# Kernel tuning notes

Measured on AMD Instinct MI355X. Metric: run time of the kernel, lower is better.

The kernel has to match this reference:

```python
import jax, jax.numpy as jnp
import numpy as np

B, S, LC, DIM, H, FFN = 1, 3600, 512, 1536, 12, 8960
HD = DIM // H          # 128
GRID = (4, 30, 30)     # f*h*w == S
K_LEN = 9900           # hardcoded k_lens in SelfAttention.forward
EPS = 1e-6

def _rope_axis_angles(n_pos, dim):
    inv = 1.0 / np.power(10000.0, np.arange(0, dim, 2, dtype=np.float64) / dim)
    return np.outer(np.arange(n_pos), inv)

def _build_rope(grid, head_dim):
    c = head_dim // 2                      # 64
    c1, c2 = c - 2 * (c // 3), c // 3      # 22, 21 (Wan 3D rope split)
    f, h, w = grid
    af = _rope_axis_angles(f, 2 * c1)
    ah = _rope_axis_angles(h, 2 * c2)
    aw = _rope_axis_angles(w, 2 * c2)
    ang = np.concatenate([
        np.broadcast_to(af[:, None, None, :], (f, h, w, c1)),
        np.broadcast_to(ah[None, :, None, :], (f, h, w, c2)),
        np.broadcast_to(aw[None, None, :, :], (f, h, w, c2)),
    ], axis=-1).reshape(f * h * w, c)
    return np.cos(ang).astype(np.float32), np.sin(ang).astype(np.float32)

def setup_inputs():
    key = jax.random.key(0)
    ks = iter(jax.random.split(key, 40))
    cos, sin = _build_rope(GRID, HD)
    inp = {
        'x': jax.random.normal(next(ks), (B, S, DIM), dtype=jnp.float32),
        'context': jax.random.normal(next(ks), (B, LC, DIM), dtype=jnp.float32),
        't_mod': 0.1 * jax.random.normal(next(ks), (B, 6, DIM), dtype=jnp.float32),
        'rope_cos': jnp.asarray(cos), 'rope_sin': jnp.asarray(sin),
        'modulation': jax.random.normal(next(ks), (1, 6, DIM), dtype=jnp.float32) / DIM ** 0.5,
    }
    for p in ('sa', 'ca'):
        for w in ('q', 'k', 'v', 'o'):
            inp[p + '_' + w + 'w'] = 0.02 * jax.random.normal(next(ks), (DIM, DIM), dtype=jnp.float32)
            inp[p + '_' + w + 'b'] = jnp.zeros((DIM,), jnp.float32)
        inp[p + '_nq'] = jnp.ones((DIM,), jnp.float32)
        inp[p + '_nk'] = jnp.ones((DIM,), jnp.float32)
    inp['n3_w'] = jnp.ones((DIM,), jnp.float32)
    inp['n3_b'] = jnp.zeros((DIM,), jnp.float32)
    inp['ffn_w1'] = 0.02 * jax.random.normal(next(ks), (DIM, FFN), dtype=jnp.float32)
    inp['ffn_b1'] = jnp.zeros((FFN,), jnp.float32)
    inp['ffn_w2'] = 0.02 * jax.random.normal(next(ks), (FFN, DIM), dtype=jnp.float32)
    inp['ffn_b2'] = jnp.zeros((DIM,), jnp.float32)
    return inp

def _rms(x, w):
    x32 = x.astype(jnp.float32)
    n = x32 * jax.lax.rsqrt(jnp.mean(x32 * x32, axis=-1, keepdims=True) + EPS)
    return n.astype(x.dtype) * w

def _ln(x, w=None, b=None):
    mu = jnp.mean(x, axis=-1, keepdims=True)
    var = jnp.mean(jnp.square(x - mu), axis=-1, keepdims=True)
    y = (x - mu) * jax.lax.rsqrt(var + EPS)
    return y if w is None else y * w + b

def _rope(x, cos, sin):
    b, s, h, d = x.shape
    x2 = x.reshape(b, s, h, d // 2, 2)
    xe, xo = x2[..., 0], x2[..., 1]
    c, sn = cos[None, :, None, :], sin[None, :, None, :]
    return jnp.stack([xe * c - xo * sn, xe * sn + xo * c], axis=-1).reshape(b, s, h, d)

def _attn(q, k, v, k_len=None):
    # q,k,v: [B,S,H,D]
    scores = jnp.einsum('bqhd,bkhd->bhqk', q, k) * (q.shape[-1] ** -0.5)
    if k_len is not None:
        mask = jnp.arange(k.shape[1]) < k_len
        scores = jnp.where(mask[None, None, None, :], scores, jnp.finfo(scores.dtype).min)
    return jnp.einsum('bhqk,bkhd->bqhd', jax.nn.softmax(scores, axis=-1), v)

def reference(x, context, t_mod, rope_cos, rope_sin, modulation,
              sa_qw, sa_qb, sa_kw, sa_kb, sa_vw, sa_vb, sa_ow, sa_ob, sa_nq, sa_nk,
              ca_qw, ca_qb, ca_kw, ca_kb, ca_vw, ca_vb, ca_ow, ca_ob, ca_nq, ca_nk,
              n3_w, n3_b, ffn_w1, ffn_b1, ffn_w2, ffn_b2):
    mod = modulation + t_mod                      # [B,6,DIM]
    sh_msa, sc_msa, g_msa, sh_mlp, sc_mlp, g_mlp = [mod[:, i:i + 1] for i in range(6)]
    b = x.shape[0]
    # --- self-attention with AdaLN modulate + 3D RoPE + k_lens mask ---
    h = _ln(x) * (1 + sc_msa) + sh_msa
    q = _rms(h @ sa_qw + sa_qb, sa_nq).reshape(b, -1, H, HD)
    k = _rms(h @ sa_kw + sa_kb, sa_nk).reshape(b, -1, H, HD)
    v = (h @ sa_vw + sa_vb).reshape(b, -1, H, HD)
    a = _attn(_rope(q, rope_cos, rope_sin), _rope(k, rope_cos, rope_sin), v, k_len=K_LEN)
    x = x + g_msa * (a.reshape(b, -1, DIM) @ sa_ow + sa_ob)
    # --- cross-attention ---
    hc = _ln(x, n3_w, n3_b)
    q = _rms(hc @ ca_qw + ca_qb, ca_nq).reshape(b, -1, H, HD)
    k = _rms(context @ ca_kw + ca_kb, ca_nk).reshape(b, -1, H, HD)
    v = (context @ ca_vw + ca_vb).reshape(b, -1, H, HD)
    x = x + (_attn(q, k, v).reshape(b, -1, DIM) @ ca_ow + ca_ob)
    # --- gated FFN with AdaLN modulate ---
    h = _ln(x) * (1 + sc_mlp) + sh_mlp
    h = jax.nn.gelu(h @ ffn_w1 + ffn_b1, approximate=True) @ ffn_w2 + ffn_b2
    return x + g_mlp * h
```

## Files before the change

kernel.cpp:

```cpp
#include <hip/hip_runtime.h>
#include <cstdint>

#define S_LEN 3600
#define DMODEL 1536
#define LCTX 512
#define NH 12
#define HDIM 128
#define FFND 8960
#define SPAD_SELF 3616

typedef short v8s __attribute__((ext_vector_type(8)));
typedef float v4f __attribute__((ext_vector_type(4)));
typedef unsigned short u16b;
typedef unsigned int u32b;

__device__ __forceinline__ u16b f2b(float f){
  union { float f; u32b i; } x; x.f = f;
  u32b r = x.i + 0x7fffu + ((x.i >> 16) & 1u);
  return (u16b)(r >> 16);
}

__device__ __forceinline__ int swz4(int row){ return (row ^ (row >> 2)) & 3; }

__global__ void add_vec(const float* __restrict__ a, const float* __restrict__ b,
                        float* __restrict__ o, int n){
  int i = blockIdx.x * 256 + threadIdx.x;
  if (i < n) o[i] = a[i] + b[i];
}

__global__ void f2b_kernel(const float* __restrict__ in, u16b* __restrict__ out, int n){
  int i = blockIdx.x * 256 + threadIdx.x;
  if (i < n) out[i] = f2b(in[i]);
}

struct WJob { const float* W; u16b* WT; int K; int N; int t0; };
struct WJobs { WJob j[10]; };

__global__ __launch_bounds__(256) void wconv(WJobs jobs){
  __shared__ float tile[32][33];
  int b = blockIdx.x;
  int ji = 0;
  #pragma unroll
  for (int i = 0; i < 10; ++i) if (b >= jobs.j[i].t0) ji = i;
  WJob jb = jobs.j[ji];
  int rel = b - jb.t0;
  int ntn = jb.N / 32;
  int k0 = (rel / ntn) * 32, n0 = (rel % ntn) * 32;
  int tx = threadIdx.x & 31, ty = threadIdx.x >> 5;
  #pragma unroll
  for (int r = ty; r < 32; r += 8) tile[r][tx] = jb.W[(size_t)(k0 + r) * jb.N + n0 + tx];
  __syncthreads();
  #pragma unroll
  for (int r = ty; r < 32; r += 8) jb.WT[(size_t)(n0 + r) * jb.K + k0 + tx] = f2b(tile[tx][r]);
}

__global__ __launch_bounds__(256) void vtrans(const u16b* __restrict__ V,
                                              u16b* __restrict__ Vt,
                                              int S, int Spad){
  __shared__ u16b t[32][136];
  int h = blockIdx.y, kb = blockIdx.x * 32, tid = threadIdx.x;
  int row = tid >> 3, ch = tid & 7;
  int key = kb + row;
  if (key < S){
    float4 a = *(const float4*)(V + (size_t)key * DMODEL + h * HDIM + ch * 16);
    float4 b = *(const float4*)(V + (size_t)key * DMODEL + h * HDIM + ch * 16 + 8);
    *(float4*)&t[row][ch * 16] = a;
    *(float4*)&t[row][ch * 16 + 8] = b;
  } else {
    float4 z = {0.f, 0.f, 0.f, 0.f};
    *(float4*)&t[row][ch * 16] = z;
    *(float4*)&t[row][ch * 16 + 8] = z;
  }
  __syncthreads();
  int hd = tid >> 1, kc = (tid & 1) * 16;
  u16b* dst = Vt + ((size_t)h * HDIM + hd) * Spad + kb + kc;
  #pragma unroll
  for (int e = 0; e < 16; e += 2){
    u32b pk = ((u32b)t[kc + e][hd]) | (((u32b)t[kc + e + 1][hd]) << 16);
    *(u32b*)(dst + e) = pk;
  }
}

__global__ __launch_bounds__(256) void ln_mod(const float* __restrict__ X,
                                              const float* __restrict__ gamma,
                                              const float* __restrict__ beta,
                                              float gadd, u16b* __restrict__ out){
  int row = blockIdx.x;
  const float* xr = X + (size_t)row * DMODEL;
  int tid = threadIdx.x;
  float v[6]; float s1 = 0.f, s2 = 0.f;
  #pragma unroll
  for (int j = 0; j < 6; ++j){ v[j] = xr[tid + j * 256]; s1 += v[j]; s2 += v[j] * v[j]; }
  #pragma unroll
  for (int o = 1; o < 64; o <<= 1){ s1 += __shfl_xor(s1, o); s2 += __shfl_xor(s2, o); }
  __shared__ float red[8];
  int wid = tid >> 6, lane = tid & 63;
  if (!lane){ red[wid * 2] = s1; red[wid * 2 + 1] = s2; }
  __syncthreads();
  s1 = red[0] + red[2] + red[4] + red[6];
  s2 = red[1] + red[3] + red[5] + red[7];
  float mu = s1 / DMODEL;
  float var = s2 / DMODEL - mu * mu;
  float rstd = rsqrtf(var + 1e-6f);
  #pragma unroll
  for (int j = 0; j < 6; ++j){
    int c = tid + j * 256;
    float g = gamma[c] + gadd;
    float b = beta[c];
    out[(size_t)row * DMODEL + c] = f2b((v[j] - mu) * rstd * g + b);
  }
}

__global__ __launch_bounds__(256) void rms_rope(const float* __restrict__ X,
                                                const float* __restrict__ w,
                                                const float* __restrict__ cosT,
                                                const float* __restrict__ sinT,
                                                u16b* __restrict__ out){
  int row = blockIdx.x;
  const float* xr = X + (size_t)row * DMODEL;
  int tid = threadIdx.x;
  float2 v[3]; float ss = 0.f;
  #pragma unroll
  for (int j = 0; j < 3; ++j){
    v[j] = *(const float2*)(xr + 2 * (tid + j * 256));
    ss += v[j].x * v[j].x + v[j].y * v[j].y;
  }
  #pragma unroll
  for (int o = 1; o < 64; o <<= 1) ss += __shfl_xor(ss, o);
  __shared__ float red[4];
  int wid = tid >> 6, lane = tid & 63;
  if (!lane) red[wid] = ss;
  __syncthreads();
  ss = red[0] + red[1] + red[2] + red[3];
  float rstd = rsqrtf(ss / DMODEL + 1e-6f);
  #pragma unroll
  for (int j = 0; j < 3; ++j){
    int p = tid + j * 256;
    float xe = v[j].x * rstd * w[2 * p];
    float xo = v[j].y * rstd * w[2 * p + 1];
    float oe, oo;
    if (cosT){
      int d = p & 63;
      float c = cosT[row * 64 + d], sn = sinT[row * 64 + d];
      oe = xe * c - xo * sn; oo = xe * sn + xo * c;
    } else { oe = xe; oo = xo; }
    u32b packed = ((u32b)f2b(oe)) | (((u32b)f2b(oo)) << 16);
    *(u32b*)(out + (size_t)row * DMODEL + 2 * p) = packed;
  }
}

template<int EPI>
__global__ __launch_bounds__(256, 2) void gemm_bt(
    const u16b* __restrict__ A, const u16b* __restrict__ BT,
    const float* __restrict__ bias, const float* __restrict__ res,
    const float* __restrict__ gate, float* __restrict__ outF,
    u16b* __restrict__ outB, int M, int N, int K)
{
  __shared__ u16b Al[128 * 32];
  __shared__ u16b Bl[128 * 32];
  const int tid = threadIdx.x, lane = tid & 63, wid = tid >> 6;
  const int bm = blockIdx.x * 128, bn = blockIdx.y * 128;
  const int wm = (wid >> 1) * 64, wn = (wid & 1) * 64;
  v4f acc[4][4] = {};
  const int g0 = tid, g1 = tid + 256;
  const int r0 = g0 >> 2, c0 = g0 & 3, r1 = g1 >> 2, c1 = g1 & 3;
  const size_t a_off0 = (size_t)min(bm + r0, M - 1) * K + c0 * 8;
  const size_t a_off1 = (size_t)min(bm + r1, M - 1) * K + c1 * 8;
  const size_t b_off0 = (size_t)(bn + r0) * K + c0 * 8;
  const size_t b_off1 = (size_t)(bn + r1) * K + c1 * 8;
  char* Ab = (char*)Al; char* Bb = (char*)Bl;
  const int wA0 = r0 * 64 + ((c0 ^ swz4(r0)) * 16);
  const int wA1 = r1 * 64 + ((c1 ^ swz4(r1)) * 16);
  float4 ra0, ra1, rb0, rb1;
  auto ldg = [&](int k0){
    ra0 = *(const float4*)(A + a_off0 + k0);
    ra1 = *(const float4*)(A + a_off1 + k0);
    rb0 = *(const float4*)(BT + b_off0 + k0);
    rb1 = *(const float4*)(BT + b_off1 + k0);
  };
  auto stw = [&](){
    *(float4*)(Ab + wA0) = ra0; *(float4*)(Ab + wA1) = ra1;
    *(float4*)(Bb + wA0) = rb0; *(float4*)(Bb + wA1) = rb1;
  };
  const int nt = K / 32;
  ldg(0); stw(); __syncthreads();
  const int chk = lane >> 4, qr = lane & 15;
  for (int t = 0; t < nt; ++t){
    if (t + 1 < nt) ldg((t + 1) * 32);
    v8s af[4], bfr[4];
    #pragma unroll
    for (int f = 0; f < 4; ++f){
      int rowa = wm + f * 16 + qr;
      af[f] = *(const v8s*)(Ab + rowa * 64 + ((chk ^ swz4(rowa)) * 16));
      int rowb = wn + f * 16 + qr;
      bfr[f] = *(const v8s*)(Bb + rowb * 64 + ((chk ^ swz4(rowb)) * 16));
    }
    #pragma unroll
    for (int i = 0; i < 4; ++i)
      #pragma unroll
      for (int j = 0; j < 4; ++j)
        acc[i][j] = __builtin_amdgcn_mfma_f32_16x16x32_bf16(af[i], bfr[j], acc[i][j], 0, 0, 0);
    __syncthreads();
    if (t + 1 < nt){ stw(); __syncthreads(); }
  }
  const int rr = lane >> 4;
  #pragma unroll
  for (int i = 0; i < 4; ++i){
    #pragma unroll
    for (int j = 0; j < 4; ++j){
      int n = bn + wn + j * 16 + qr;
      float bv = bias ? bias[n] : 0.f;
      float gv = (EPI == 2 && gate) ? gate[n] : 1.f;
      #pragma unroll
      for (int r = 0; r < 4; ++r){
        int m = bm + wm + i * 16 + rr * 4 + r;
        if (m < M){
          float val = acc[i][j][r] + bv;
          size_t idx = (size_t)m * N + n;
          if (EPI == 0) outB[idx] = f2b(val);
          else if (EPI == 1) outF[idx] = val;
          else if (EPI == 2) outF[idx] = res[idx] + gv * val;
          else {
            float t3 = val * val * val;
            float th = tanhf(0.7978845608028654f * (val + 0.044715f * t3));
            outB[idx] = f2b(0.5f * val * (1.f + th));
          }
        }
      }
    }
  }
}

__global__ __launch_bounds__(256, 2) void flash_attn(
    const u16b* __restrict__ Q, const u16b* __restrict__ Kp,
    const u16b* __restrict__ Vt, u16b* __restrict__ O,
    int Sq, int Sk, int Spad)
{
  __shared__ u16b Klds[32 * 128];
  __shared__ u16b Vlds[128 * 32];
  __shared__ u16b Plds[4 * 16 * 32];
  const int tid = threadIdx.x, lane = tid & 63, wid = tid >> 6;
  const int h = blockIdx.y;
  const int q0 = blockIdx.x * 64 + wid * 16;
  const int qq = lane & 15, cc = lane >> 4;
  char* Kb = (char*)Klds; char* Vb = (char*)Vlds; char* Pb = (char*)Plds;

  v8s qf[4];
  {
    int qrow = min(q0 + qq, Sq - 1);
    const u16b* qp = Q + (size_t)qrow * DMODEL + h * HDIM + cc * 8;
    #pragma unroll
    for (int ks = 0; ks < 4; ++ks) qf[ks] = *(const v8s*)(qp + ks * 32);
  }
  float mrun = -1e30f, lrun = 0.f;
  v4f oacc[8] = {};
  const float scale = 0.08838834764831845f;

  for (int kb0 = 0; kb0 < Sk; kb0 += 32){
    __syncthreads();
    #pragma unroll
    for (int c = 0; c < 2; ++c){
      int g = tid + c * 256;
      int krow = g >> 4, kgc = g & 15;
      int key = min(kb0 + krow, Sk - 1);
      *(float4*)(Kb + krow * 256 + ((kgc ^ (krow & 7)) * 16)) =
          *(const float4*)(Kp + (size_t)key * DMODEL + h * HDIM + kgc * 8);
      int vr = g >> 2, vc = g & 3;
      *(float4*)(Vb + vr * 64 + ((vc ^ swz4(vr)) * 16)) =
          *(const float4*)(Vt + ((size_t)h * HDIM + vr) * Spad + kb0 + vc * 8);
    }
    __syncthreads();

    float s[8];
    #pragma unroll
    for (int sub = 0; sub < 2; ++sub){
      v4f sa = {0.f, 0.f, 0.f, 0.f};
      #pragma unroll
      for (int ks = 0; ks < 4; ++ks){
        int row = sub * 16 + qq;
        v8s kf = *(const v8s*)(Kb + row * 256 + (((ks * 4 + cc) ^ (row & 7)) * 16));
        sa = __builtin_amdgcn_mfma_f32_16x16x32_bf16(kf, qf[ks], sa, 0, 0, 0);
      }
      #pragma unroll
      for (int r = 0; r < 4; ++r) s[sub * 4 + r] = sa[r] * scale;
    }
    if (kb0 + 32 > Sk){
      #pragma unroll
      for (int i = 0; i < 8; ++i){
        int key = kb0 + (i >> 2) * 16 + cc * 4 + (i & 3);
        if (key >= Sk) s[i] = -1e30f;
      }
    }
    float cmax = s[0];
    #pragma unroll
    for (int i = 1; i < 8; ++i) cmax = fmaxf(cmax, s[i]);
    cmax = fmaxf(cmax, __shfl_xor(cmax, 16));
    cmax = fmaxf(cmax, __shfl_xor(cmax, 32));
    float mnew = fmaxf(mrun, cmax);
    float alpha = __expf(mrun - mnew);
    mrun = mnew;
    float p[8]; float csum = 0.f;
    #pragma unroll
    for (int i = 0; i < 8; ++i){ p[i] = __expf(s[i] - mnew); csum += p[i]; }
    csum += __shfl_xor(csum, 16);
    csum += __shfl_xor(csum, 32);
    lrun = lrun * alpha + csum;

    #pragma unroll
    for (int sub = 0; sub < 2; ++sub){
      int key0 = sub * 16 + cc * 4;
      u32b u01 = ((u32b)f2b(p[sub * 4 + 0])) | (((u32b)f2b(p[sub * 4 + 1])) << 16);
      u32b u23 = ((u32b)f2b(p[sub * 4 + 2])) | (((u32b)f2b(p[sub * 4 + 3])) << 16);
      char* base = Pb + wid * 1024 + qq * 64 + (((key0 >> 3) ^ ((qq >> 1) & 3)) * 16) + (key0 & 7) * 2;
      *(u32b*)base = u01;
      *(u32b*)(base + 4) = u23;
    }
    float alr[4];
    #pragma unroll
    for (int r = 0; r < 4; ++r) alr[r] = __shfl(alpha, cc * 4 + r);
    #pragma unroll
    for (int f = 0; f < 8; ++f)
      #pragma unroll
      for (int r = 0; r < 4; ++r) oacc[f][r] *= alr[r];

    v8s pf = *(const v8s*)(Pb + wid * 1024 + qq * 64 + ((cc ^ ((qq >> 1) & 3)) * 16));

    #pragma unroll
    for (int hdb = 0; hdb < 8; ++hdb){
      int row = hdb * 16 + qq;
      v8s vf = *(const v8s*)(Vb + row * 64 + ((cc ^ swz4(row)) * 16));
      oacc[hdb] = __builtin_amdgcn_mfma_f32_16x16x32_bf16(pf, vf, oacc[hdb], 0, 0, 0);
    }
  }

  float linv = 1.f / lrun;
  float lr[4];
  #pragma unroll
  for (int r = 0; r < 4; ++r) lr[r] = __shfl(linv, cc * 4 + r);
  #pragma unroll
  for (int hdb = 0; hdb < 8; ++hdb)
    #pragma unroll
    for (int r = 0; r < 4; ++r){
      int qrow = q0 + cc * 4 + r;
      if (qrow < Sq)
        O[(size_t)qrow * DMODEL + h * HDIM + hdb * 16 + qq] = f2b(oacc[hdb][r] * lr[r]);
    }
}

extern "C" void kernel_launch(void* const* d_in, const int* in_sizes, int n_in,
                              void* d_out, int out_size, void* d_ws, size_t ws_size,
                              hipStream_t stream){
  (void)in_sizes; (void)n_in; (void)out_size; (void)ws_size;
  const float* x     = (const float*)d_in[0];
  const float* ctx   = (const float*)d_in[1];
  const float* t_mod = (const float*)d_in[2];
  const float* ropec = (const float*)d_in[3];
  const float* ropes = (const float*)d_in[4];
  const float* modu  = (const float*)d_in[5];
  const float* sa_qw = (const float*)d_in[6];  const float* sa_qb = (const float*)d_in[7];
  const float* sa_kw = (const float*)d_in[8];  const float* sa_kb = (const float*)d_in[9];
  const float* sa_vw = (const float*)d_in[10]; const float* sa_vb = (const float*)d_in[11];
  const float* sa_ow = (const float*)d_in[12]; const float* sa_ob = (const float*)d_in[13];
  const float* sa_nq = (const float*)d_in[14]; const float* sa_nk = (const float*)d_in[15];
  const float* ca_qw = (const float*)d_in[16]; const float* ca_qb = (const float*)d_in[17];
  const float* ca_kw = (const float*)d_in[18]; const float* ca_kb = (const float*)d_in[19];
  const float* ca_vw = (const float*)d_in[20]; const float* ca_vb = (const float*)d_in[21];
  const float* ca_ow = (const float*)d_in[22]; const float* ca_ob = (const float*)d_in[23];
  const float* ca_nq = (const float*)d_in[24]; const float* ca_nk = (const float*)d_in[25];
  const float* n3w   = (const float*)d_in[26]; const float* n3b   = (const float*)d_in[27];
  const float* fw1   = (const float*)d_in[28]; const float* fb1   = (const float*)d_in[29];
  const float* fw2   = (const float*)d_in[30]; const float* fb2   = (const float*)d_in[31];
  float* out = (float*)d_out;

  char* wsp = (char*)d_ws;
  size_t off = 0;
  auto alloc = [&](size_t b){ void* p = wsp + off; off += (b + 255) & ~(size_t)255; return p; };
  const size_t WW = (size_t)DMODEL * DMODEL * 2;
  float* modc = (float*)alloc(6 * DMODEL * 4);
  u16b* w1T   = (u16b*)alloc((size_t)FFND * DMODEL * 2);
  u16b* w2T   = (u16b*)alloc((size_t)DMODEL * FFND * 2);
  u16b* h_bf  = (u16b*)alloc((size_t)S_LEN * DMODEL * 2);
  float* pre0 = (float*)alloc((size_t)S_LEN * DMODEL * 4);
  size_t region0 = off;
  u16b* sa_qwT = (u16b*)alloc(WW);
  u16b* sa_kwT = (u16b*)alloc(WW);
  u16b* sa_vwT = (u16b*)alloc(WW);
  u16b* sa_owT = (u16b*)alloc(WW);
  u16b* ca_qwT = (u16b*)alloc(WW);
  u16b* ca_kwT = (u16b*)alloc(WW);
  u16b* ca_vwT = (u16b*)alloc(WW);
  u16b* ca_owT = (u16b*)alloc(WW);
  float* x2    = (float*)alloc((size_t)S_LEN * DMODEL * 4);
  float* pre2  = (float*)alloc((size_t)LCTX * DMODEL * 4);
  u16b* qb     = (u16b*)alloc((size_t)S_LEN * DMODEL * 2);
  u16b* kb     = (u16b*)alloc((size_t)S_LEN * DMODEL * 2);
  u16b* vb     = (u16b*)alloc((size_t)S_LEN * DMODEL * 2);
  u16b* ab     = (u16b*)alloc((size_t)S_LEN * DMODEL * 2);
  u16b* ctxb   = (u16b*)alloc((size_t)LCTX * DMODEL * 2);
  u16b* k2b    = (u16b*)alloc((size_t)LCTX * DMODEL * 2);
  u16b* v2b    = (u16b*)alloc((size_t)LCTX * DMODEL * 2);
  u16b* vts    = (u16b*)alloc((size_t)NH * HDIM * SPAD_SELF * 2);
  u16b* vtc    = (u16b*)alloc((size_t)NH * HDIM * LCTX * 2);
  u16b* fmid = (u16b*)(wsp + region0);

  add_vec<<<36, 256, 0, stream>>>(modu, t_mod, modc, 6 * DMODEL);

  WJobs jobs; int t = 0;
  auto addjob = [&](int i, const float* w_, u16b* wt, int K, int N){
    jobs.j[i].W = w_; jobs.j[i].WT = wt; jobs.j[i].K = K; jobs.j[i].N = N; jobs.j[i].t0 = t;
    t += (K / 32) * (N / 32);
  };
  addjob(0, sa_qw, sa_qwT, DMODEL, DMODEL);
  addjob(1, sa_kw, sa_kwT, DMODEL, DMODEL);
  addjob(2, sa_vw, sa_vwT, DMODEL, DMODEL);
  addjob(3, sa_ow, sa_owT, DMODEL, DMODEL);
  addjob(4, ca_qw, ca_qwT, DMODEL, DMODEL);
  addjob(5, ca_kw, ca_kwT, DMODEL, DMODEL);
  addjob(6, ca_vw, ca_vwT, DMODEL, DMODEL);
  addjob(7, ca_ow, ca_owT, DMODEL, DMODEL);
  addjob(8, fw1, w1T, DMODEL, FFND);
  addjob(9, fw2, w2T, FFND, DMODEL);
  wconv<<<t, 256, 0, stream>>>(jobs);

  f2b_kernel<<<(LCTX * DMODEL) / 256, 256, 0, stream>>>(ctx, ctxb, LCTX * DMODEL);

  ln_mod<<<S_LEN, 256, 0, stream>>>(x, modc + DMODEL, modc, 1.f, h_bf);
  dim3 g12(29, 12), g42(4, 12);
  gemm_bt<1><<<g12, 256, 0, stream>>>(h_bf, sa_qwT, sa_qb, nullptr, nullptr, pre0, nullptr, S_LEN, DMODEL, DMODEL);
  gemm_bt<1><<<g12, 256, 0, stream>>>(h_bf, sa_kwT, sa_kb, nullptr, nullptr, x2, nullptr, S_LEN, DMODEL, DMODEL);
  gemm_bt<0><<<g12, 256, 0, stream>>>(h_bf, sa_vwT, sa_vb, nullptr, nullptr, nullptr, vb, S_LEN, DMODEL, DMODEL);
  rms_rope<<<S_LEN, 256, 0, stream>>>(pre0, sa_nq, ropec, ropes, qb);
  rms_rope<<<S_LEN, 256, 0, stream>>>(x2, sa_nk, ropec, ropes, kb);
  vtrans<<<dim3(113, 12), 256, 0, stream>>>(vb, vts, S_LEN, SPAD_SELF);
  flash_attn<<<dim3(57, 12), 256, 0, stream>>>(qb, kb, vts, ab, S_LEN, S_LEN, SPAD_SELF);
  gemm_bt<2><<<g12, 256, 0, stream>>>(ab, sa_owT, sa_ob, x, modc + 2 * DMODEL, x2, nullptr, S_LEN, DMODEL, DMODEL);

  ln_mod<<<S_LEN, 256, 0, stream>>>(x2, n3w, n3b, 0.f, h_bf);
  gemm_bt<1><<<g12, 256, 0, stream>>>(h_bf, ca_qwT, ca_qb, nullptr, nullptr, pre0, nullptr, S_LEN, DMODEL, DMODEL);
  gemm_bt<1><<<g42, 256, 0, stream>>>(ctxb, ca_kwT, ca_kb, nullptr, nullptr, pre2, nullptr, LCTX, DMODEL, DMODEL);
  gemm_bt<0><<<g42, 256, 0, stream>>>(ctxb, ca_vwT, ca_vb, nullptr, nullptr, nullptr, v2b, LCTX, DMODEL, DMODEL);
  rms_rope<<<S_LEN, 256, 0, stream>>>(pre0, ca_nq, nullptr, nullptr, qb);
  rms_rope<<<LCTX, 256, 0, stream>>>(pre2, ca_nk, nullptr, nullptr, k2b);
  vtrans<<<dim3(16, 12), 256, 0, stream>>>(v2b, vtc, LCTX, LCTX);
  flash_attn<<<dim3(57, 12), 256, 0, stream>>>(qb, k2b, vtc, ab, S_LEN, LCTX, LCTX);
  gemm_bt<2><<<g12, 256, 0, stream>>>(ab, ca_owT, ca_ob, x2, nullptr, pre0, nullptr, S_LEN, DMODEL, DMODEL);

  ln_mod<<<S_LEN, 256, 0, stream>>>(pre0, modc + 4 * DMODEL, modc + 3 * DMODEL, 1.f, h_bf);
  gemm_bt<3><<<dim3(29, 70), 256, 0, stream>>>(h_bf, w1T, fb1, nullptr, nullptr, nullptr, fmid, S_LEN, FFND, DMODEL);
  gemm_bt<2><<<g12, 256, 0, stream>>>(fmid, w2T, fb2, pre0, modc + 5 * DMODEL, out, nullptr, S_LEN, DMODEL, FFND);
}
```

Before: 1.104 ms.

## Fuse QKV GEMMs, split-K FFN2, widen flash-attn tiles with prefetch and lazy rescale

The self-attention Q/K/V projections now run as one segmented GEMM over concatenated transposed weights, and the cross-attention K/V projections are merged the same way. The FFN down-projection is split along K into two partial GEMMs followed by a reduce kernel that applies bias, gate and residual, so the narrow N=1536 grid gets more blocks. Flash attention moves to 64-key tiles with register prefetch of the next K/V tile and skips the online-softmax rescale unless the running max grows by more than a threshold. MFMA sections are wrapped in s_setprio, and SPAD is raised to a multiple of 64. These changes add LDS use and a partial-sum buffer, and the lazy rescale trades a little exp headroom for fewer multiplies.

```diff
diff --git a/kernel.cpp b/kernel.cpp
--- a/kernel.cpp
+++ b/kernel.cpp
@@ -7,7 +7,7 @@
 #define NH 12
 #define HDIM 128
 #define FFND 8960
-#define SPAD_SELF 3616
+#define SPAD_SELF 3648
 
 typedef short v8s __attribute__((ext_vector_type(8)));
 typedef float v4f __attribute__((ext_vector_type(4)));
@@ -154,7 +154,93 @@
     const u16b* __restrict__ A, const u16b* __restrict__ BT,
     const float* __restrict__ bias, const float* __restrict__ res,
     const float* __restrict__ gate, float* __restrict__ outF,
-    u16b* __restrict__ outB, int M, int N, int K)
+    u16b* __restrict__ outB, int M, int N, int K, int kLen)
+{
+  __shared__ u16b Al[128 * 32];
+  __shared__ u16b Bl[128 * 32];
+  const int tid = threadIdx.x, lane = tid & 63, wid = tid >> 6;
+  const int bm = blockIdx.x * 128, bn = blockIdx.y * 128;
+  const int kbase = blockIdx.z * kLen;
+  const int wm = (wid >> 1) * 64, wn = (wid & 1) * 64;
+  v4f acc[4][4] = {};
+  const int g0 = tid, g1 = tid + 256;
+  const int r0 = g0 >> 2, c0 = g0 & 3, r1 = g1 >> 2, c1 = g1 & 3;
+  const size_t a_off0 = (size_t)min(bm + r0, M - 1) * K + kbase + c0 * 8;
+  const size_t a_off1 = (size_t)min(bm + r1, M - 1) * K + kbase + c1 * 8;
+  const size_t b_off0 = (size_t)(bn + r0) * K + kbase + c0 * 8;
+  const size_t b_off1 = (size_t)(bn + r1) * K + kbase + c1 * 8;
+  char* Ab = (char*)Al; char* Bb = (char*)Bl;
+  const int wA0 = r0 * 64 + ((c0 ^ swz4(r0)) * 16);
+  const int wA1 = r1 * 64 + ((c1 ^ swz4(r1)) * 16);
+  float4 ra0, ra1, rb0, rb1;
+  auto ldg = [&](int k0){
+    ra0 = *(const float4*)(A + a_off0 + k0);
+    ra1 = *(const float4*)(A + a_off1 + k0);
+    rb0 = *(const float4*)(BT + b_off0 + k0);
+    rb1 = *(const float4*)(BT + b_off1 + k0);
+  };
+  auto stw = [&](){
+    *(float4*)(Ab + wA0) = ra0; *(float4*)(Ab + wA1) = ra1;
+    *(float4*)(Bb + wA0) = rb0; *(float4*)(Bb + wA1) = rb1;
+  };
+  const int nt = kLen / 32;
+  ldg(0); stw(); __syncthreads();
+  const int chk = lane >> 4, qr = lane & 15;
+  for (int t = 0; t < nt; ++t){
+    if (t + 1 < nt) ldg((t + 1) * 32);
+    v8s af[4], bfr[4];
+    #pragma unroll
+    for (int f = 0; f < 4; ++f){
+      int rowa = wm + f * 16 + qr;
+      af[f] = *(const v8s*)(Ab + rowa * 64 + ((chk ^ swz4(rowa)) * 16));
+      int rowb = wn + f * 16 + qr;
+      bfr[f] = *(const v8s*)(Bb + rowb * 64 + ((chk ^ swz4(rowb)) * 16));
+    }
+    __builtin_amdgcn_s_setprio(1);
+    #pragma unroll
+    for (int i = 0; i < 4; ++i)
+      #pragma unroll
+      for (int j = 0; j < 4; ++j)
+        acc[i][j] = __builtin_amdgcn_mfma_f32_16x16x32_bf16(af[i], bfr[j], acc[i][j], 0, 0, 0);
+    __builtin_amdgcn_s_setprio(0);
+    __syncthreads();
+    if (t + 1 < nt){ stw(); __syncthreads(); }
+  }
+  const int rr = lane >> 4;
+  #pragma unroll
+  for (int i = 0; i < 4; ++i){
+    #pragma unroll
+    for (int j = 0; j < 4; ++j){
+      int n = bn + wn + j * 16 + qr;
+      float bv = (EPI != 5 && bias) ? bias[n] : 0.f;
+      float gv = (EPI == 2 && gate) ? gate[n] : 1.f;
+      #pragma unroll
+      for (int r = 0; r < 4; ++r){
+        int m = bm + wm + i * 16 + rr * 4 + r;
+        if (m < M){
+          float val = acc[i][j][r] + bv;
+          size_t idx = (size_t)m * N + n;
+          if (EPI == 0) outB[idx] = f2b(val);
+          else if (EPI == 1) outF[idx] = val;
+          else if (EPI == 2) outF[idx] = res[idx] + gv * val;
+          else if (EPI == 5) outF[(size_t)blockIdx.z * M * N + idx] = val;
+          else {
+            float t3 = val * val * val;
+            float th = tanhf(0.7978845608028654f * (val + 0.044715f * t3));
+            outB[idx] = f2b(0.5f * val * (1.f + th));
+          }
+        }
+      }
+    }
+  }
+}
+
+struct Seg { const float* bias; float* outF; u16b* outB; };
+struct Segs { Seg s[3]; };
+
+__global__ __launch_bounds__(256, 2) void gemm_seg(
+    const u16b* __restrict__ A, const u16b* __restrict__ BT,
+    Segs segs, int M, int N, int K)
 {
   __shared__ u16b Al[128 * 32];
   __shared__ u16b Bl[128 * 32];
@@ -195,40 +281,59 @@
       int rowb = wn + f * 16 + qr;
       bfr[f] = *(const v8s*)(Bb + rowb * 64 + ((chk ^ swz4(rowb)) * 16));
     }
+    __builtin_amdgcn_s_setprio(1);
     #pragma unroll
     for (int i = 0; i < 4; ++i)
       #pragma unroll
       for (int j = 0; j < 4; ++j)
         acc[i][j] = __builtin_amdgcn_mfma_f32_16x16x32_bf16(af[i], bfr[j], acc[i][j], 0, 0, 0);
+    __builtin_amdgcn_s_setprio(0);
     __syncthreads();
     if (t + 1 < nt){ stw(); __syncthreads(); }
   }
+  const int seg = bn / 1536;
+  const Seg sg = segs.s[seg];
   const int rr = lane >> 4;
   #pragma unroll
   for (int i = 0; i < 4; ++i){
     #pragma unroll
     for (int j = 0; j < 4; ++j){
-      int n = bn + wn + j * 16 + qr;
-      float bv = bias ? bias[n] : 0.f;
-      float gv = (EPI == 2 && gate) ? gate[n] : 1.f;
+      int nloc = bn - seg * 1536 + wn + j * 16 + qr;
+      float bv = sg.bias[nloc];
       #pragma unroll
       for (int r = 0; r < 4; ++r){
         int m = bm + wm + i * 16 + rr * 4 + r;
         if (m < M){
           float val = acc[i][j][r] + bv;
-          size_t idx = (size_t)m * N + n;
-          if (EPI == 0) outB[idx] = f2b(val);
-          else if (EPI == 1) outF[idx] = val;
-          else if (EPI == 2) outF[idx] = res[idx] + gv * val;
-          else {
-            float t3 = val * val * val;
-            float th = tanhf(0.7978845608028654f * (val + 0.044715f * t3));
-            outB[idx] = f2b(0.5f * val * (1.f + th));
-          }
+          size_t idx = (size_t)m * 1536 + nloc;
+          if (sg.outB) sg.outB[idx] = f2b(val);
+          else sg.outF[idx] = val;
         }
       }
     }
   }
+}
+
+__global__ __launch_bounds__(256) void ffn2_reduce(const float* __restrict__ part,
+                                                   const float* __restrict__ res,
+                                                   const float* __restrict__ bias,
+                                                   const float* __restrict__ gate,
+                                                   float* __restrict__ out, int total){
+  int i4 = blockIdx.x * 256 + threadIdx.x;
+  if (i4 * 4 >= total) return;
+  int base = i4 * 4;
+  int n = base % DMODEL;
+  float4 p0 = *(const float4*)(part + base);
+  float4 p1 = *(const float4*)(part + (size_t)total + base);
+  float4 rs = *(const float4*)(res + base);
+  float4 bv = *(const float4*)(bias + n);
+  float4 gv = *(const float4*)(gate + n);
+  float4 o;
+  o.x = rs.x + gv.x * (p0.x + p1.x + bv.x);
+  o.y = rs.y + gv.y * (p0.y + p1.y + bv.y);
+  o.z = rs.z + gv.z * (p0.z + p1.z + bv.z);
+  o.w = rs.w + gv.w * (p0.w + p1.w + bv.w);
+  *(float4*)(out + base) = o;
 }
 
 __global__ __launch_bounds__(256, 2) void flash_attn(
@@ -236,14 +341,15 @@
     const u16b* __restrict__ Vt, u16b* __restrict__ O,
     int Sq, int Sk, int Spad)
 {
-  __shared__ u16b Klds[32 * 128];
-  __shared__ u16b Vlds[128 * 32];
-  __shared__ u16b Plds[4 * 16 * 32];
+  __shared__ u16b Klds[64 * 128];
+  __shared__ u16b Vlds[128 * 64];
+  __shared__ u16b Plds[4 * 16 * 64];
   const int tid = threadIdx.x, lane = tid & 63, wid = tid >> 6;
   const int h = blockIdx.y;
   const int q0 = blockIdx.x * 64 + wid * 16;
   const int qq = lane & 15, cc = lane >> 4;
-  char* Kb = (char*)Klds; char* Vb = (char*)Vlds; char* Pb = (char*)Plds;
+  char* Kb = (char*)Klds; char* Vb = (char*)Vlds;
+  char* Pb = (char*)Plds + wid * 2048;
 
   v8s qf[4];
   {
@@ -255,82 +361,103 @@
   float mrun = -1e30f, lrun = 0.f;
   v4f oacc[8] = {};
   const float scale = 0.08838834764831845f;
-
-  for (int kb0 = 0; kb0 < Sk; kb0 += 32){
-    __syncthreads();
-    #pragma unroll
-    for (int c = 0; c < 2; ++c){
+  const int nt = (Sk + 63) >> 6;
+
+  float4 rk[4], rv[4];
+  auto ldg = [&](int kb0){
+    #pragma unroll
+    for (int c = 0; c < 4; ++c){
       int g = tid + c * 256;
       int krow = g >> 4, kgc = g & 15;
       int key = min(kb0 + krow, Sk - 1);
-      *(float4*)(Kb + krow * 256 + ((kgc ^ (krow & 7)) * 16)) =
-          *(const float4*)(Kp + (size_t)key * DMODEL + h * HDIM + kgc * 8);
-      int vr = g >> 2, vc = g & 3;
-      *(float4*)(Vb + vr * 64 + ((vc ^ swz4(vr)) * 16)) =
-          *(const float4*)(Vt + ((size_t)h * HDIM + vr) * Spad + kb0 + vc * 8);
-    }
-    __syncthreads();
-
-    float s[8];
-    #pragma unroll
-    for (int sub = 0; sub < 2; ++sub){
+      rk[c] = *(const float4*)(Kp + (size_t)key * DMODEL + h * HDIM + kgc * 8);
+      int vr = g >> 3, vc = g & 7;
+      rv[c] = *(const float4*)(Vt + ((size_t)h * HDIM + vr) * Spad + kb0 + vc * 8);
+    }
+  };
+  auto stw = [&](){
+    #pragma unroll
+    for (int c = 0; c < 4; ++c){
+      int g = tid + c * 256;
+      int krow = g >> 4, kgc = g & 15;
+      *(float4*)(Kb + krow * 256 + ((kgc ^ (krow & 7)) * 16)) = rk[c];
+      int vr = g >> 3, vc = g & 7;
+      *(float4*)(Vb + vr * 128 + ((vc ^ (vr & 7)) * 16)) = rv[c];
+    }
+  };
+  ldg(0); stw(); __syncthreads();
+
+  for (int t = 0; t < nt; ++t){
+    int kb0 = t << 6;
+    if (t + 1 < nt) ldg(kb0 + 64);
+    float s[16];
+    __builtin_amdgcn_s_setprio(1);
+    #pragma unroll
+    for (int sub = 0; sub < 4; ++sub){
       v4f sa = {0.f, 0.f, 0.f, 0.f};
+      int row = sub * 16 + qq;
       #pragma unroll
       for (int ks = 0; ks < 4; ++ks){
-        int row = sub * 16 + qq;
         v8s kf = *(const v8s*)(Kb + row * 256 + (((ks * 4 + cc) ^ (row & 7)) * 16));
         sa = __builtin_amdgcn_mfma_f32_16x16x32_bf16(kf, qf[ks], sa, 0, 0, 0);
       }
       #pragma unroll
       for (int r = 0; r < 4; ++r) s[sub * 4 + r] = sa[r] * scale;
     }
-    if (kb0 + 32 > Sk){
-      #pragma unroll
-      for (int i = 0; i < 8; ++i){
+    __builtin_amdgcn_s_setprio(0);
+    if (kb0 + 64 > Sk){
+      #pragma unroll
+      for (int i = 0; i < 16; ++i){
         int key = kb0 + (i >> 2) * 16 + cc * 4 + (i & 3);
         if (key >= Sk) s[i] = -1e30f;
       }
     }
-    float cmax = s[0];
-    #pragma unroll
-    for (int i = 1; i < 8; ++i) cmax = fmaxf(cmax, s[i]);
-    cmax = fmaxf(cmax, __shfl_xor(cmax, 16));
-    cmax = fmaxf(cmax, __shfl_xor(cmax, 32));
-    float mnew = fmaxf(mrun, cmax);
-    float alpha = __expf(mrun - mnew);
-    mrun = mnew;
-    float p[8]; float csum = 0.f;
-    #pragma unroll
-    for (int i = 0; i < 8; ++i){ p[i] = __expf(s[i] - mnew); csum += p[i]; }
+    float pmax = s[0];
+    #pragma unroll
+    for (int i = 1; i < 16; ++i) pmax = fmaxf(pmax, s[i]);
+    pmax = fmaxf(pmax, __shfl_xor(pmax, 16));
+    pmax = fmaxf(pmax, __shfl_xor(pmax, 32));
+    if (!__all(pmax <= mrun + 8.f)){
+      float mnew = fmaxf(mrun, pmax);
+      float alpha = __expf(mrun - mnew);
+      mrun = mnew;
+      float alr[4];
+      #pragma unroll
+      for (int r = 0; r < 4; ++r) alr[r] = __shfl(alpha, cc * 4 + r);
+      #pragma unroll
+      for (int f = 0; f < 8; ++f)
+        #pragma unroll
+        for (int r = 0; r < 4; ++r) oacc[f][r] *= alr[r];
+      lrun *= alpha;
+    }
+    float p[16]; float csum = 0.f;
+    #pragma unroll
+    for (int i = 0; i < 16; ++i){ p[i] = __expf(s[i] - mrun); csum += p[i]; }
     csum += __shfl_xor(csum, 16);
     csum += __shfl_xor(csum, 32);
-    lrun = lrun * alpha + csum;
-
-    #pragma unroll
-    for (int sub = 0; sub < 2; ++sub){
-      int key0 = sub * 16 + cc * 4;
+    lrun += csum;
+    #pragma unroll
+    for (int sub = 0; sub < 4; ++sub){
       u32b u01 = ((u32b)f2b(p[sub * 4 + 0])) | (((u32b)f2b(p[sub * 4 + 1])) << 16);
       u32b u23 = ((u32b)f2b(p[sub * 4 + 2])) | (((u32b)f2b(p[sub * 4 + 3])) << 16);
-      char* base = Pb + wid * 1024 + qq * 64 + (((key0 >> 3) ^ ((qq >> 1) & 3)) * 16) + (key0 & 7) * 2;
-      *(u32b*)base = u01;
-      *(u32b*)(base + 4) = u23;
-    }
-    float alr[4];
-    #pragma unroll
-    for (int r = 0; r < 4; ++r) alr[r] = __shfl(alpha, cc * 4 + r);
-    #pragma unroll
-    for (int f = 0; f < 8; ++f)
-      #pragma unroll
-      for (int r = 0; r < 4; ++r) oacc[f][r] *= alr[r];
-
-    v8s pf = *(const v8s*)(Pb + wid * 1024 + qq * 64 + ((cc ^ ((qq >> 1) & 3)) * 16));
-
+      int gI = sub * 2 + (cc >> 1);
+      uint2 w2; w2.x = u01; w2.y = u23;
+      *(uint2*)(Pb + qq * 128 + ((gI ^ (qq & 7)) * 16) + (cc & 1) * 8) = w2;
+    }
+    v8s pf0 = *(const v8s*)(Pb + qq * 128 + (((cc) ^ (qq & 7)) * 16));
+    v8s pf1 = *(const v8s*)(Pb + qq * 128 + (((4 + cc) ^ (qq & 7)) * 16));
+    __builtin_amdgcn_s_setprio(1);
     #pragma unroll
     for (int hdb = 0; hdb < 8; ++hdb){
       int row = hdb * 16 + qq;
-      v8s vf = *(const v8s*)(Vb + row * 64 + ((cc ^ swz4(row)) * 16));
-      oacc[hdb] = __builtin_amdgcn_mfma_f32_16x16x32_bf16(pf, vf, oacc[hdb], 0, 0, 0);
-    }
+      v8s vf0 = *(const v8s*)(Vb + row * 128 + (((cc) ^ (row & 7)) * 16));
+      v8s vf1 = *(const v8s*)(Vb + row * 128 + (((4 + cc) ^ (row & 7)) * 16));
+      oacc[hdb] = __builtin_amdgcn_mfma_f32_16x16x32_bf16(pf0, vf0, oacc[hdb], 0, 0, 0);
+      oacc[hdb] = __builtin_amdgcn_mfma_f32_16x16x32_bf16(pf1, vf1, oacc[hdb], 0, 0, 0);
+    }
+    __builtin_amdgcn_s_setprio(0);
+    __syncthreads();
+    if (t + 1 < nt){ stw(); __syncthreads(); }
   }
 
   float linv = 1.f / lrun;
@@ -382,14 +509,11 @@
   u16b* h_bf  = (u16b*)alloc((size_t)S_LEN * DMODEL * 2);
   float* pre0 = (float*)alloc((size_t)S_LEN * DMODEL * 4);
   size_t region0 = off;
-  u16b* sa_qwT = (u16b*)alloc(WW);
-  u16b* sa_kwT = (u16b*)alloc(WW);
-  u16b* sa_vwT = (u16b*)alloc(WW);
-  u16b* sa_owT = (u16b*)alloc(WW);
-  u16b* ca_qwT = (u16b*)alloc(WW);
-  u16b* ca_kwT = (u16b*)alloc(WW);
-  u16b* ca_vwT = (u16b*)alloc(WW);
-  u16b* ca_owT = (u16b*)alloc(WW);
+  u16b* sa_qkvT = (u16b*)alloc(3 * WW);
+  u16b* sa_owT  = (u16b*)alloc(WW);
+  u16b* ca_qwT  = (u16b*)alloc(WW);
+  u16b* ca_kvT  = (u16b*)alloc(2 * WW);
+  u16b* ca_owT  = (u16b*)alloc(WW);
   float* x2    = (float*)alloc((size_t)S_LEN * DMODEL * 4);
   float* pre2  = (float*)alloc((size_t)LCTX * DMODEL * 4);
   u16b* qb     = (u16b*)alloc((size_t)S_LEN * DMODEL * 2);
@@ -402,6 +526,7 @@
   u16b* vts    = (u16b*)alloc((size_t)NH * HDIM * SPAD_SELF * 2);
   u16b* vtc    = (u16b*)alloc((size_t)NH * HDIM * LCTX * 2);
   u16b* fmid = (u16b*)(wsp + region0);
+  float* fpart = (float*)(wsp + region0 + (size_t)S_LEN * FFND * 2);
 
   add_vec<<<36, 256, 0, stream>>>(modu, t_mod, modc, 6 * DMODEL);
 
@@ -410,42 +535,56 @@
     jobs.j[i].W = w_; jobs.j[i].WT = wt; jobs.j[i].K = K; jobs.j[i].N = N; jobs.j[i].t0 = t;
     t += (K / 32) * (N / 32);
   };
-  addjob(0, sa_qw, sa_qwT, DMODEL, DMODEL);
-  addjob(1, sa_kw, sa_kwT, DMODEL, DMODEL);
-  addjob(2, sa_vw, sa_vwT, DMODEL, DMODEL);
+  addjob(0, sa_qw, sa_qkvT,           DMODEL, DMODEL);
+  addjob(1, sa_kw, sa_qkvT + WW,      DMODEL, DMODEL);
+  addjob(2, sa_vw, sa_qkvT + WW,      DMODEL, DMODEL);
   addjob(3, sa_ow, sa_owT, DMODEL, DMODEL);
   addjob(4, ca_qw, ca_qwT, DMODEL, DMODEL);
-  addjob(5, ca_kw, ca_kwT, DMODEL, DMODEL);
-  addjob(6, ca_vw, ca_vwT, DMODEL, DMODEL);
+  addjob(5, ca_kw, ca_kvT, DMODEL, DMODEL);
+  addjob(6, ca_vw, ca_kvT, DMODEL, DMODEL);
   addjob(7, ca_ow, ca_owT, DMODEL, DMODEL);
   addjob(8, fw1, w1T, DMODEL, FFND);
   addjob(9, fw2, w2T, FFND, DMODEL);
+  jobs.j[1].WT = sa_qkvT + (size_t)DMODEL * DMODEL;
+  jobs.j[2].WT = sa_qkvT + (size_t)2 * DMODEL * DMODEL;
+  jobs.j[5].WT = ca_kvT;
+  jobs.j[6].WT = ca_kvT + (size_t)DMODEL * DMODEL;
   wconv<<<t, 256, 0, stream>>>(jobs);
 
   f2b_kernel<<<(LCTX * DMODEL) / 256, 256, 0, stream>>>(ctx, ctxb, LCTX * DMODEL);
 
   ln_mod<<<S_LEN, 256, 0, stream>>>(x, modc + DMODEL, modc, 1.f, h_bf);
   dim3 g12(29, 12), g42(4, 12);
-  gemm_bt<1><<<g12, 256, 0, stream>>>(h_bf, sa_qwT, sa_qb, nullptr, nullptr, pre0, nullptr, S_LEN, DMODEL, DMODEL);
-  gemm_bt<1><<<g12, 256, 0, stream>>>(h_bf, sa_kwT, sa_kb, nullptr, nullptr, x2, nullptr, S_LEN, DMODEL, DMODEL);
-  gemm_bt<0><<<g12, 256, 0, stream>>>(h_bf, sa_vwT, sa_vb, nullptr, nullptr, nullptr, vb, S_LEN, DMODEL, DMODEL);
+  {
+    Segs sg;
+    sg.s[0] = { sa_qb, pre0, nullptr };
+    sg.s[1] = { sa_kb, x2,   nullptr };
+    sg.s[2] = { sa_vb, nullptr, vb   };
+    gemm_seg<<<dim3(29, 36), 256, 0, stream>>>(h_bf, sa_qkvT, sg, S_LEN, 3 * DMODEL, DMODEL);
+  }
   rms_rope<<<S_LEN, 256, 0, stream>>>(pre0, sa_nq, ropec, ropes, qb);
   rms_rope<<<S_LEN, 256, 0, stream>>>(x2, sa_nk, ropec, ropes, kb);
-  vtrans<<<dim3(113, 12), 256, 0, stream>>>(vb, vts, S_LEN, SPAD_SELF);
+  vtrans<<<dim3(SPAD_SELF / 32, 12), 256, 0, stream>>>(vb, vts, S_LEN, SPAD_SELF);
   flash_attn<<<dim3(57, 12), 256, 0, stream>>>(qb, kb, vts, ab, S_LEN, S_LEN, SPAD_SELF);
-  gemm_bt<2><<<g12, 256, 0, stream>>>(ab, sa_owT, sa_ob, x, modc + 2 * DMODEL, x2, nullptr, S_LEN, DMODEL, DMODEL);
+  gemm_bt<2><<<g12, 256, 0, stream>>>(ab, sa_owT, sa_ob, x, modc + 2 * DMODEL, x2, nullptr, S_LEN, DMODEL, DMODEL, DMODEL);
 
   ln_mod<<<S_LEN, 256, 0, stream>>>(x2, n3w, n3b, 0.f, h_bf);
-  gemm_bt<1><<<g12, 256, 0, stream>>>(h_bf, ca_qwT, ca_qb, nullptr, nullptr, pre0, nullptr, S_LEN, DMODEL, DMODEL);
-  gemm_bt<1><<<g42, 256, 0, stream>>>(ctxb, ca_kwT, ca_kb, nullptr, nullptr, pre2, nullptr, LCTX, DMODEL, DMODEL);
-  gemm_bt<0><<<g42, 256, 0, stream>>>(ctxb, ca_vwT, ca_vb, nullptr, nullptr, nullptr, v2b, LCTX, DMODEL, DMODEL);
+  gemm_bt<1><<<g12, 256, 0, stream>>>(h_bf, ca_qwT, ca_qb, nullptr, nullptr, pre0, nullptr, S_LEN, DMODEL, DMODEL, DMODEL);
+  {
+    Segs sg;
+    sg.s[0] = { ca_kb, pre2, nullptr };
+    sg.s[1] = { ca_vb, nullptr, v2b  };
+    sg.s[2] = { ca_vb, nullptr, v2b  };
+    gemm_seg<<<dim3(4, 24), 256, 0, stream>>>(ctxb, ca_kvT, sg, LCTX, 2 * DMODEL, DMODEL);
+  }
   rms_rope<<<S_LEN, 256, 0, stream>>>(pre0, ca_nq, nullptr, nullptr, qb);
   rms_rope<<<LCTX, 256, 0, stream>>>(pre2, ca_nk, nullptr, nullptr, k2b);
   vtrans<<<dim3(16, 12), 256, 0, stream>>>(v2b, vtc, LCTX, LCTX);
   flash_attn<<<dim3(57, 12), 256, 0, stream>>>(qb, k2b, vtc, ab, S_LEN, LCTX, LCTX);
-  gemm_bt<2><<<g12, 256, 0, stream>>>(ab, ca_owT, ca_ob, x2, nullptr, pre0, nullptr, S_LEN, DMODEL, DMODEL);
+  gemm_bt<2><<<g12, 256, 0, stream>>>(ab, ca_owT, ca_ob, x2, nullptr, pre0, nullptr, S_LEN, DMODEL, DMODEL, DMODEL);
 
   ln_mod<<<S_LEN, 256, 0, stream>>>(pre0, modc + 4 * DMODEL, modc + 3 * DMODEL, 1.f, h_bf);
-  gemm_bt<3><<<dim3(29, 70), 256, 0, stream>>>(h_bf, w1T, fb1, nullptr, nullptr, nullptr, fmid, S_LEN, FFND, DMODEL);
-  gemm_bt<2><<<g12, 256, 0, stream>>>(fmid, w2T, fb2, pre0, modc + 5 * DMODEL, out, nullptr, S_LEN, DMODEL, FFND);
-}
+  gemm_bt<3><<<dim3(29, 70), 256, 0, stream>>>(h_bf, w1T, fb1, nullptr, nullptr, nullptr, fmid, S_LEN, FFND, DMODEL, DMODEL);
+  gemm_bt<5><<<dim3(29, 12, 2), 256, 0, stream>>>(fmid, w2T, nullptr, nullptr, nullptr, fpart, nullptr, S_LEN, DMODEL, FFND, FFND / 2);
+  ffn2_reduce<<<(S_LEN * DMODEL / 4 + 255) / 256, 256, 0, stream>>>(fpart, pre0, fb2, modc + 5 * DMODEL, out, S_LEN * DMODEL);
+}
```

Result: slower. 1.280 ms (+15.9%).
